# Optimization experiments

Hardware: AMD Instinct MI355X
Metric: run time of the kernel (lower is better)

## Reference

```python
import jax, jax.numpy as jnp
import numpy as np

E, D, H, O, K = 8, 1024, 4096, 1024, 2
N = 4096


def setup_inputs() -> dict:
    key = jax.random.key(0)
    ks = jax.random.split(key, 8)
    s_in = 1.0 / np.sqrt(D)
    s_h = 1.0 / np.sqrt(H)
    return {
        "x": jax.random.normal(ks[0], (N, D), dtype=jnp.float32),
        "W1": jax.random.uniform(ks[1], (E, D, H), jnp.float32, -s_in, s_in),
        "b1": jax.random.uniform(ks[2], (E, H), jnp.float32, -s_in, s_in),
        "W2": jax.random.uniform(ks[3], (E, H, O), jnp.float32, -s_h, s_h),
        "b2": jax.random.uniform(ks[4], (E, O), jnp.float32, -s_h, s_h),
        "Wg": jax.random.uniform(ks[5], (D, E), jnp.float32, -s_in, s_in),
        "bg": jax.random.uniform(ks[6], (E,), jnp.float32, -s_in, s_in),
    }


def reference(x, W1, b1, W2, b2, Wg, bg):
    # gate: [N, E] -> top-k logits and expert ids
    gate_logits = x @ Wg + bg
    topv, topi = jax.lax.top_k(gate_logits, K)          # [N, K]
    weights = jax.nn.softmax(topv, axis=-1)             # softmax over the k selected logits

    # dense all-expert MLP, then gather the selected experts per token
    h = jax.nn.relu(jnp.einsum("nd,edh->enh", x, W1) + b1[:, None, :])  # [E, N, H]
    y = jnp.einsum("enh,eho->eno", h, W2) + b2[:, None, :]              # [E, N, O]

    sel = y[topi, jnp.arange(N)[:, None]]               # [N, K, O]
    return jnp.sum(weights[..., None] * sel, axis=1)    # [N, O]
```

## Files before the change

kernel.cpp:

```cpp
#include <hip/hip_runtime.h>
#include <hip/hip_bf16.h>
#include <cstdint>

typedef __bf16 bf16;
typedef bf16 bf16x8 __attribute__((ext_vector_type(8)));
typedef bf16 bf16x4 __attribute__((ext_vector_type(4)));
typedef float f32x4 __attribute__((ext_vector_type(4)));

#define N_TOK 4096
#define DIM   1024
#define HID   4096
#define OUTD  1024
#define NEXP  8

__device__ __forceinline__ void async_copy16(const void* g, void* l) {
  __builtin_amdgcn_global_load_lds(
      (const __attribute__((address_space(1))) void*)g,
      (__attribute__((address_space(3))) void*)l, 16, 0, 0);
}

__global__ __launch_bounds__(256) void gate_kernel(
    const float* __restrict__ x, const float* __restrict__ Wg,
    const float* __restrict__ bg, int* __restrict__ topE, float* __restrict__ topW)
{
  int wave = threadIdx.x >> 6, lane = threadIdx.x & 63;
  int t = blockIdx.x * 4 + wave;
  float acc[8];
#pragma unroll
  for (int e = 0; e < 8; ++e) acc[e] = 0.f;
  const float* xrow = x + (size_t)t * DIM;
#pragma unroll
  for (int i = 0; i < DIM / 64; ++i) {
    int d = i * 64 + lane;
    float xv = xrow[d];
    float4 w0 = *(const float4*)(Wg + d * 8);
    float4 w1 = *(const float4*)(Wg + d * 8 + 4);
    acc[0] += xv * w0.x; acc[1] += xv * w0.y; acc[2] += xv * w0.z; acc[3] += xv * w0.w;
    acc[4] += xv * w1.x; acc[5] += xv * w1.y; acc[6] += xv * w1.z; acc[7] += xv * w1.w;
  }
#pragma unroll
  for (int off = 32; off > 0; off >>= 1) {
#pragma unroll
    for (int e = 0; e < 8; ++e) acc[e] += __shfl_xor(acc[e], off, 64);
  }
  if (lane == 0) {
    float l[8];
#pragma unroll
    for (int e = 0; e < 8; ++e) l[e] = acc[e] + bg[e];
    int e1 = 0;
#pragma unroll
    for (int e = 1; e < 8; ++e) if (l[e] > l[e1]) e1 = e;
    int e2 = (e1 == 0) ? 1 : 0;
#pragma unroll
    for (int e = 0; e < 8; ++e) if (e != e1 && l[e] > l[e2]) e2 = e;
    float w1 = 1.f / (1.f + __expf(l[e2] - l[e1]));
    topE[t * 2] = e1; topE[t * 2 + 1] = e2;
    topW[t * 2] = w1; topW[t * 2 + 1] = 1.f - w1;
  }
}

__global__ __launch_bounds__(256) void build_lists(
    const int* __restrict__ topE, const float* __restrict__ topW,
    int* __restrict__ cnt, int* __restrict__ tok_list, float* __restrict__ w_list)
{
  __shared__ int lcnt[8], lbase[8];
  int tid = threadIdx.x;
  if (tid < 8) lcnt[tid] = 0;
  __syncthreads();
  int t = blockIdx.x * 256 + tid;
  int e1 = topE[2 * t], e2 = topE[2 * t + 1];
  float w1 = topW[2 * t], w2 = topW[2 * t + 1];
  int p1 = atomicAdd(&lcnt[e1], 1);
  int p2 = atomicAdd(&lcnt[e2], 1);
  __syncthreads();
  if (tid < 8) lbase[tid] = atomicAdd(&cnt[tid], lcnt[tid]);
  __syncthreads();
  int i1 = e1 * N_TOK + lbase[e1] + p1;
  int i2 = e2 * N_TOK + lbase[e2] + p2;
  tok_list[i1] = t; w_list[i1] = w1;
  tok_list[i2] = t; w_list[i2] = w2;
}

__global__ void scan_kernel(const int* __restrict__ cnt, int* __restrict__ base)
{
  if (threadIdx.x == 0) {
    int s = 0;
    for (int e = 0; e < 8; ++e) { base[e] = s; s += cnt[e]; }
    base[8] = s;
  }
}

__global__ __launch_bounds__(256) void gather_cvt(
    const float* __restrict__ x, const int* __restrict__ tok_list,
    const int* __restrict__ base, bf16* __restrict__ xg)
{
  int wave = threadIdx.x >> 6, lane = threadIdx.x & 63;
  int s = blockIdx.x * 4 + wave;
  int e = 0;
#pragma unroll
  for (int i = 1; i < 8; ++i) e += (s >= base[i]);
  int tok = tok_list[e * N_TOK + (s - base[e])];
  const float4* src = (const float4*)(x + (size_t)tok * DIM);
  bf16x4* dst = (bf16x4*)(xg + (size_t)s * DIM);
#pragma unroll
  for (int i = 0; i < DIM / 256; ++i) {
    float4 v = src[i * 64 + lane];
    bf16x4 o;
    o.x = (bf16)v.x; o.y = (bf16)v.y; o.z = (bf16)v.z; o.w = (bf16)v.w;
    dst[i * 64 + lane] = o;
  }
}

__global__ __launch_bounds__(256) void transpose_cvt(
    const float* __restrict__ src, bf16* __restrict__ dst, int R, int C)
{
  __shared__ bf16 tile[64][65];
  int e = blockIdx.z;
  const float* s = src + (size_t)e * R * C;
  bf16* d = dst + (size_t)e * R * C;
  int c0 = blockIdx.x * 64, r0 = blockIdx.y * 64;
  int tr = threadIdx.x >> 6, tc = threadIdx.x & 63;
#pragma unroll
  for (int i = 0; i < 16; ++i) {
    int r = i * 4 + tr;
    tile[r][tc] = (bf16)s[(size_t)(r0 + r) * C + c0 + tc];
  }
  __syncthreads();
#pragma unroll
  for (int i = 0; i < 16; ++i) {
    int rt = i * 4 + tr;
    d[(size_t)(c0 + rt) * R + r0 + tc] = tile[tc][rt];
  }
}

__global__ __launch_bounds__(256) void gemm1_kernel(
    const bf16* __restrict__ xg, const bf16* __restrict__ W1t,
    const float* __restrict__ b1, bf16* __restrict__ hbuf,
    const int* __restrict__ cnt, const int* __restrict__ base)
{
  int e = blockIdx.z;
  int M = cnt[e];
  int mt = blockIdx.y;
  if (mt * 128 >= M) return;
  int nt = blockIdx.x;
  int b0 = base[e];

  __shared__ bf16 As[128 * 32];
  __shared__ bf16 Bs[128 * 32];

  int tid = threadIdx.x;
  int wave = tid >> 6, lane = tid & 63;

  int rA0 = wave * 32 + (lane >> 2);
  int rA1 = rA0 + 16;
  int kofs = (lane & 3) * 8;
  int lm0 = min(mt * 128 + rA0, M - 1);
  int lm1 = min(mt * 128 + rA1, M - 1);
  const bf16* gA0 = xg + (size_t)(b0 + lm0) * DIM + kofs;
  const bf16* gA1 = xg + (size_t)(b0 + lm1) * DIM + kofs;
  const bf16* gB0 = W1t + ((size_t)e * HID + nt * 128 + rA0) * DIM + kofs;
  const bf16* gB1 = W1t + ((size_t)e * HID + nt * 128 + rA1) * DIM + kofs;
  bf16* lA0 = As + (wave * 2 + 0) * 512;
  bf16* lA1 = As + (wave * 2 + 1) * 512;
  bf16* lB0 = Bs + (wave * 2 + 0) * 512;
  bf16* lB1 = Bs + (wave * 2 + 1) * 512;

  int wm = wave & 1, wn = wave >> 1;
  int quad = lane >> 4, lr = lane & 15;
  f32x4 acc[4][4] = {};

  for (int kt = 0; kt < DIM / 32; ++kt) {
    int ko = kt * 32;
    async_copy16(gA0 + ko, lA0);
    async_copy16(gA1 + ko, lA1);
    async_copy16(gB0 + ko, lB0);
    async_copy16(gB1 + ko, lB1);
    __syncthreads();
    bf16x8 af[4], bfr[4];
#pragma unroll
    for (int i = 0; i < 4; ++i)
      af[i] = *(const bf16x8*)(As + (wm * 64 + i * 16 + lr) * 32 + quad * 8);
#pragma unroll
    for (int j = 0; j < 4; ++j)
      bfr[j] = *(const bf16x8*)(Bs + (wn * 64 + j * 16 + lr) * 32 + quad * 8);
#pragma unroll
    for (int i = 0; i < 4; ++i)
#pragma unroll
      for (int j = 0; j < 4; ++j)
        acc[i][j] = __builtin_amdgcn_mfma_f32_16x16x32_bf16(af[i], bfr[j], acc[i][j], 0, 0, 0);
    __syncthreads();
  }

#pragma unroll
  for (int j = 0; j < 4; ++j) {
    int col = nt * 128 + wn * 64 + j * 16 + lr;
    float bias = b1[e * HID + col];
#pragma unroll
    for (int i = 0; i < 4; ++i) {
#pragma unroll
      for (int r = 0; r < 4; ++r) {
        int lm = mt * 128 + wm * 64 + i * 16 + quad * 4 + r;
        if (lm < M) {
          float v = acc[i][j][r] + bias;
          hbuf[(size_t)(b0 + lm) * HID + col] = (bf16)fmaxf(v, 0.f);
        }
      }
    }
  }
}

__global__ __launch_bounds__(256) void gemm2_kernel(
    const bf16* __restrict__ hbuf, const bf16* __restrict__ W2t,
    const float* __restrict__ b2, float* __restrict__ out,
    const int* __restrict__ cnt, const int* __restrict__ base,
    const int* __restrict__ tok_list, const float* __restrict__ w_list)
{
  int e = blockIdx.z;
  int M = cnt[e];
  int mt = blockIdx.y;
  if (mt * 128 >= M) return;
  int nt = blockIdx.x;
  int b0 = base[e];

  __shared__ bf16 As[128 * 32];
  __shared__ bf16 Bs[128 * 32];

  int tid = threadIdx.x;
  int wave = tid >> 6, lane = tid & 63;

  int rA0 = wave * 32 + (lane >> 2);
  int rA1 = rA0 + 16;
  int kofs = (lane & 3) * 8;
  int lm0 = min(mt * 128 + rA0, M - 1);
  int lm1 = min(mt * 128 + rA1, M - 1);
  const bf16* gA0 = hbuf + (size_t)(b0 + lm0) * HID + kofs;
  const bf16* gA1 = hbuf + (size_t)(b0 + lm1) * HID + kofs;
  const bf16* gB0 = W2t + ((size_t)e * OUTD + nt * 128 + rA0) * HID + kofs;
  const bf16* gB1 = W2t + ((size_t)e * OUTD + nt * 128 + rA1) * HID + kofs;
  bf16* lA0 = As + (wave * 2 + 0) * 512;
  bf16* lA1 = As + (wave * 2 + 1) * 512;
  bf16* lB0 = Bs + (wave * 2 + 0) * 512;
  bf16* lB1 = Bs + (wave * 2 + 1) * 512;

  int wm = wave & 1, wn = wave >> 1;
  int quad = lane >> 4, lr = lane & 15;
  f32x4 acc[4][4] = {};

  for (int kt = 0; kt < HID / 32; ++kt) {
    int ko = kt * 32;
    async_copy16(gA0 + ko, lA0);
    async_copy16(gA1 + ko, lA1);
    async_copy16(gB0 + ko, lB0);
    async_copy16(gB1 + ko, lB1);
    __syncthreads();
    bf16x8 af[4], bfr[4];
#pragma unroll
    for (int i = 0; i < 4; ++i)
      af[i] = *(const bf16x8*)(As + (wm * 64 + i * 16 + lr) * 32 + quad * 8);
#pragma unroll
    for (int j = 0; j < 4; ++j)
      bfr[j] = *(const bf16x8*)(Bs + (wn * 64 + j * 16 + lr) * 32 + quad * 8);
#pragma unroll
    for (int i = 0; i < 4; ++i)
#pragma unroll
      for (int j = 0; j < 4; ++j)
        acc[i][j] = __builtin_amdgcn_mfma_f32_16x16x32_bf16(af[i], bfr[j], acc[i][j], 0, 0, 0);
    __syncthreads();
  }

#pragma unroll
  for (int i = 0; i < 4; ++i) {
#pragma unroll
    for (int r = 0; r < 4; ++r) {
      int lm = mt * 128 + wm * 64 + i * 16 + quad * 4 + r;
      if (lm < M) {
        int tok = tok_list[e * N_TOK + lm];
        float w = w_list[e * N_TOK + lm];
#pragma unroll
        for (int j = 0; j < 4; ++j) {
          int col = nt * 128 + wn * 64 + j * 16 + lr;
          float v = acc[i][j][r] + b2[e * OUTD + col];
          atomicAdd(out + (size_t)tok * OUTD + col, w * v);
        }
      }
    }
  }
}

extern "C" void kernel_launch(void* const* d_in, const int* in_sizes, int n_in,
                              void* d_out, int out_size, void* d_ws, size_t ws_size,
                              hipStream_t stream)
{
  (void)in_sizes; (void)n_in; (void)ws_size;
  const float* x  = (const float*)d_in[0];
  const float* W1 = (const float*)d_in[1];
  const float* b1 = (const float*)d_in[2];
  const float* W2 = (const float*)d_in[3];
  const float* b2 = (const float*)d_in[4];
  const float* Wg = (const float*)d_in[5];
  const float* bg = (const float*)d_in[6];
  float* out = (float*)d_out;

  char* ws = (char*)d_ws;
  int*   tok_list = (int*)(ws + 0);
  float* w_list   = (float*)(ws + 131072);
  int*   topE     = (int*)(ws + 262144);
  float* topW     = (float*)(ws + 294912);
  int*   cnt      = (int*)(ws + 327680);
  int*   base     = (int*)(ws + 327744);
  bf16*  xg   = (bf16*)(ws + 393216);
  bf16*  W1t  = (bf16*)(ws + 17170432);
  bf16*  hbuf = (bf16*)(ws + 84279296);
  bf16*  W2t  = (bf16*)(ws + 393216);

  hipMemsetAsync(d_out, 0, (size_t)out_size * sizeof(float), stream);
  hipMemsetAsync(cnt, 0, 64, stream);

  gate_kernel<<<dim3(N_TOK / 4), 256, 0, stream>>>(x, Wg, bg, topE, topW);
  build_lists<<<dim3(N_TOK / 256), 256, 0, stream>>>(topE, topW, cnt, tok_list, w_list);
  scan_kernel<<<dim3(1), 64, 0, stream>>>(cnt, base);
  gather_cvt<<<dim3(2 * N_TOK / 4), 256, 0, stream>>>(x, tok_list, base, xg);
  transpose_cvt<<<dim3(HID / 64, DIM / 64, NEXP), 256, 0, stream>>>(W1, W1t, DIM, HID);
  gemm1_kernel<<<dim3(HID / 128, N_TOK / 128, NEXP), 256, 0, stream>>>(xg, W1t, b1, hbuf, cnt, base);
  transpose_cvt<<<dim3(OUTD / 64, HID / 64, NEXP), 256, 0, stream>>>(W2, W2t, HID, OUTD);
  gemm2_kernel<<<dim3(OUTD / 128, N_TOK / 128, NEXP), 256, 0, stream>>>(hbuf, W2t, b2, out, cnt, base, tok_list, w_list);
}
```

Before: 604.5 us.

## Split-K the second expert GEMM and vectorize the weight transpose

The second grouped GEMM now splits the hidden dimension into four chunks across extra grid blocks. Each chunk accumulates its partial product into the output through the existing atomic adds, and only the first chunk adds the bias. This raises parallelism for the low-occupancy gemm2, whose grid has only 8 N-tiles per expert, at the cost of four times as many atomic adds on the output. The transpose-convert kernel also switches to float4 loads and bf16x4 stores to cut the number of memory transactions, though the LDS writes now access the tile with strided, column-wise addresses.

Result: slower. 680.3 us (+12.5%).

```diff
diff --git a/kernel.cpp b/kernel.cpp
--- a/kernel.cpp
+++ b/kernel.cpp
@@ -12,6 +12,7 @@
 #define HID   4096
 #define OUTD  1024
 #define NEXP  8
+#define KSPLIT 4
 
 __device__ __forceinline__ void async_copy16(const void* g, void* l) {
   __builtin_amdgcn_global_load_lds(
@@ -119,17 +120,28 @@
   const float* s = src + (size_t)e * R * C;
   bf16* d = dst + (size_t)e * R * C;
   int c0 = blockIdx.x * 64, r0 = blockIdx.y * 64;
-  int tr = threadIdx.x >> 6, tc = threadIdx.x & 63;
-#pragma unroll
-  for (int i = 0; i < 16; ++i) {
-    int r = i * 4 + tr;
-    tile[r][tc] = (bf16)s[(size_t)(r0 + r) * C + c0 + tc];
+  int tid = threadIdx.x;
+  int rr = tid >> 4;
+  int cc = (tid & 15) * 4;
+#pragma unroll
+  for (int i = 0; i < 4; ++i) {
+    int r = i * 16 + rr;
+    float4 v = *(const float4*)(s + (size_t)(r0 + r) * C + c0 + cc);
+    tile[cc + 0][r] = (bf16)v.x;
+    tile[cc + 1][r] = (bf16)v.y;
+    tile[cc + 2][r] = (bf16)v.z;
+    tile[cc + 3][r] = (bf16)v.w;
   }
   __syncthreads();
 #pragma unroll
-  for (int i = 0; i < 16; ++i) {
-    int rt = i * 4 + tr;
-    d[(size_t)(c0 + rt) * R + r0 + tc] = tile[tc][rt];
+  for (int i = 0; i < 4; ++i) {
+    int ct = i * 16 + rr;
+    bf16x4 o;
+    o.x = tile[ct][cc + 0];
+    o.y = tile[ct][cc + 1];
+    o.z = tile[ct][cc + 2];
+    o.w = tile[ct][cc + 3];
+    *(bf16x4*)(d + (size_t)(c0 + ct) * R + r0 + cc) = o;
   }
 }
 
@@ -215,12 +227,16 @@
     const int* __restrict__ cnt, const int* __restrict__ base,
     const int* __restrict__ tok_list, const float* __restrict__ w_list)
 {
-  int e = blockIdx.z;
+  int ez = blockIdx.z;
+  int e = ez / KSPLIT;
+  int ks = ez % KSPLIT;
   int M = cnt[e];
   int mt = blockIdx.y;
   if (mt * 128 >= M) return;
   int nt = blockIdx.x;
   int b0 = base[e];
+  const int KC = HID / KSPLIT;
+  int k0 = ks * KC;
 
   __shared__ bf16 As[128 * 32];
   __shared__ bf16 Bs[128 * 32];
@@ -233,10 +249,10 @@
   int kofs = (lane & 3) * 8;
   int lm0 = min(mt * 128 + rA0, M - 1);
   int lm1 = min(mt * 128 + rA1, M - 1);
-  const bf16* gA0 = hbuf + (size_t)(b0 + lm0) * HID + kofs;
-  const bf16* gA1 = hbuf + (size_t)(b0 + lm1) * HID + kofs;
-  const bf16* gB0 = W2t + ((size_t)e * OUTD + nt * 128 + rA0) * HID + kofs;
-  const bf16* gB1 = W2t + ((size_t)e * OUTD + nt * 128 + rA1) * HID + kofs;
+  const bf16* gA0 = hbuf + (size_t)(b0 + lm0) * HID + k0 + kofs;
+  const bf16* gA1 = hbuf + (size_t)(b0 + lm1) * HID + k0 + kofs;
+  const bf16* gB0 = W2t + ((size_t)e * OUTD + nt * 128 + rA0) * HID + k0 + kofs;
+  const bf16* gB1 = W2t + ((size_t)e * OUTD + nt * 128 + rA1) * HID + k0 + kofs;
   bf16* lA0 = As + (wave * 2 + 0) * 512;
   bf16* lA1 = As + (wave * 2 + 1) * 512;
   bf16* lB0 = Bs + (wave * 2 + 0) * 512;
@@ -246,7 +262,7 @@
   int quad = lane >> 4, lr = lane & 15;
   f32x4 acc[4][4] = {};
 
-  for (int kt = 0; kt < HID / 32; ++kt) {
+  for (int kt = 0; kt < KC / 32; ++kt) {
     int ko = kt * 32;
     async_copy16(gA0 + ko, lA0);
     async_copy16(gA1 + ko, lA1);
@@ -279,7 +295,8 @@
 #pragma unroll
         for (int j = 0; j < 4; ++j) {
           int col = nt * 128 + wn * 64 + j * 16 + lr;
-          float v = acc[i][j][r] + b2[e * OUTD + col];
+          float v = acc[i][j][r];
+          if (ks == 0) v += b2[e * OUTD + col];
           atomicAdd(out + (size_t)tok * OUTD + col, w * v);
         }
       }
@@ -323,5 +340,5 @@
   transpose_cvt<<<dim3(HID / 64, DIM / 64, NEXP), 256, 0, stream>>>(W1, W1t, DIM, HID);
   gemm1_kernel<<<dim3(HID / 128, N_TOK / 128, NEXP), 256, 0, stream>>>(xg, W1t, b1, hbuf, cnt, base);
   transpose_cvt<<<dim3(OUTD / 64, HID / 64, NEXP), 256, 0, stream>>>(W2, W2t, HID, OUTD);
-  gemm2_kernel<<<dim3(OUTD / 128, N_TOK / 128, NEXP), 256, 0, stream>>>(hbuf, W2t, b2, out, cnt, base, tok_list, w_list);
-}
+  gemm2_kernel<<<dim3(OUTD / 128, N_TOK / 128, NEXP * KSPLIT), 256, 0, stream>>>(hbuf, W2t, b2, out, cnt, base, tok_list, w_list);
+}
```
